# Optimization experiments

Measured on AMD Instinct MI355X. Metric: run time of the kernel, lower is better.

Reference implementation:

```python
import jax, jax.numpy as jnp
import numpy as np

N = 128       # n_channels
B = 131072    # batch
C = np.float32(np.sqrt(0.5))  # 50/50 beamsplitter amplitude (c = s = sqrt(0.5))


def setup_inputs() -> dict:
    key = jax.random.key(0)
    k1, k2, k3, k4 = jax.random.split(key, 4)
    M = N * (N - 1) // 2
    return {
        "x_real": jax.random.normal(k1, (B, N), jnp.float32),
        "x_imag": jax.random.normal(k2, (B, N), jnp.float32),
        "mzi_phases": jax.random.normal(k3, (M * 2,), jnp.float32) * 0.1,
        "output_phases": jax.random.normal(k4, (N,), jnp.float32) * 0.1,
    }


def _construct_unitary(mzi_phases, output_phases):
    n = output_phases.shape[0]
    m = n * (n - 1) // 2
    # pair ordering matches the torch double loop: i ascending, then j > i (row-major triu)
    i_np, j_np = np.triu_indices(n, 1)
    i_idx = jnp.asarray(i_np, jnp.int32)
    j_idx = jnp.asarray(j_np, jnp.int32)
    ph = mzi_phases.reshape(m, 2)
    theta, phi = ph[:, 0], ph[:, 1]

    def step(U, xs):
        th, ph_, i, j = xs
        e_phi = jax.lax.complex(jnp.cos(ph_), jnp.sin(ph_))
        e_th = jax.lax.complex(jnp.cos(th), jnp.sin(th))
        ri = U[i]
        rj = U[j]
        # T_ij @ U touches only rows i and j (O(N) Givens row update)
        new_i = C * ri + (C * e_phi) * rj
        new_j = (C * e_th) * ri - (C * e_th * e_phi) * rj
        U = U.at[i].set(new_i).at[j].set(new_j)
        return U, None

    def chunk_body(U, xs_chunk):
        U, _ = jax.lax.scan(step, U, xs_chunk)
        return U, None

    # chunk the M sequential updates: M = (n-1) * (n//2) for even n;
    # checkpointing chunks keeps reverse-mode memory O(sqrt-ish) instead of O(M * N^2)
    n_chunks = n - 1
    cs = n // 2
    xs = (theta.reshape(n_chunks, cs), phi.reshape(n_chunks, cs),
          i_idx.reshape(n_chunks, cs), j_idx.reshape(n_chunks, cs))
    U0 = jnp.eye(n, dtype=jnp.complex64)
    U, _ = jax.lax.scan(jax.checkpoint(chunk_body), U0, xs)
    # output phase screen D @ U
    d = jax.lax.complex(jnp.cos(output_phases), jnp.sin(output_phases))
    return d[:, None] * U


def reference(x_real, x_imag, mzi_phases, output_phases):
    U = _construct_unitary(mzi_phases, output_phases)           # [N, N] complex64
    x = jax.lax.complex(x_real, x_imag)                          # [B, N] complex64
    # matmul(U, x.unsqueeze(-1)).squeeze(-1) == x @ U^T
    out = jnp.einsum('nm,bm->bn', U, x)                          # [B, N] complex64
    # ComplexDropout is identity in eval mode
    return out
```

## Files before the change

kernel.cpp:

```cpp
#include <hip/hip_runtime.h>
#include <hip/hip_bf16.h>

#define NDIM 128
#define BDIM 131072
#define NMZI 8128
#define NCHUNK 8
#define CSTEP (NMZI / NCHUNK)
#define NJG 8
#define NCOL 32
#define NLOC 16
static constexpr float CC = 0.70710678118654752440f;

typedef __attribute__((ext_vector_type(8))) short bf16x8;
typedef __attribute__((ext_vector_type(4))) float f32x4;

__device__ __align__(16) float4         g_ph[NMZI];
__device__ __align__(8)  float2         g_dt[NDIM];
__device__ __align__(16) float2         g_V[NCHUNK * NDIM * NDIM];
__device__ __align__(16) float2         g_W[4 * NDIM * NDIM];
__device__ __align__(16) float2         g_Y[2 * NDIM * NDIM];
__device__ __align__(16) unsigned short g_Ur[16 * NDIM * 8];
__device__ __align__(16) unsigned short g_Ui[16 * NDIM * 8];

__device__ inline unsigned short f2bf(float f) {
    union { __hip_bfloat16 h; unsigned short u; } cv;
    cv.h = __float2bfloat16(f);
    return cv.u;
}

__global__ void phase_prep(const float* __restrict__ mzi,
                           const float* __restrict__ oph) {
    int q = blockIdx.x * blockDim.x + threadIdx.x;
    if (q < NMZI) {
        float th = mzi[2 * q];
        float p  = mzi[2 * q + 1];
        float sp, cp, st, ct;
        sincosf(p,  &sp, &cp);
        sincosf(th, &st, &ct);
        g_ph[q] = make_float4(cp, sp, CC * ct, CC * st);
    } else if (q < NMZI + NDIM) {
        int n = q - NMZI;
        float s, c;
        sincosf(oph[n], &s, &c);
        g_dt[n] = make_float2(c, s);
    }
}

__global__ __launch_bounds__(256) void build_scan() {
    __shared__ float2 Usm[NDIM][NCOL];
    __shared__ float4 phs[CSTEP];
    __shared__ float4 comp[NJG][NCOL];
    const int tid   = threadIdx.x;
    const int c     = tid & 31;
    const int g     = tid >> 5;
    const int col0  = blockIdx.x * NCOL;
    const int chunk = blockIdx.y;
    const int s0 = chunk * CSTEP, s1 = s0 + CSTEP;

    for (int k = g; k < NDIM; k += NJG)
        Usm[k][c] = make_float2((k == col0 + c) ? 1.f : 0.f, 0.f);
    for (int t = tid; t < CSTEP; t += 256) phs[t] = g_ph[s0 + t];
    __syncthreads();

    int i = 0, base = 0;
    while (base + (NDIM - 1 - i) <= s0) { base += NDIM - 1 - i; ++i; }

    int s = s0;
    while (s < s1) {
        const int cnt  = NDIM - 1 - i;
        const int jA   = i + 1 + (s - base);
        const int L    = min(s1, base + cnt) - s;
        const int nloc = (L + NJG - 1) >> 3;
        const int myBeg = g * nloc;
        const int myN   = max(0, min(nloc, L - myBeg));
        const int pbase = s - s0;

        const float2 r0 = Usm[i][c];

        float2 treg[NLOC];
        float2 qth[NLOC];
        float  A = 1.f;
        float2 Bc = make_float2(0.f, 0.f);
        #pragma unroll
        for (int kk = 0; kk < NLOC; ++kk) {
            if (kk < myN) {
                const int off = myBeg + kk;
                const float4 q  = phs[pbase + off];
                const float2 rj = Usm[jA + off][c];
                const float tr = fmaf(q.x, rj.x, -q.y * rj.y);
                const float ti = fmaf(q.x, rj.y,  q.y * rj.x);
                treg[kk] = make_float2(tr, ti);
                qth[kk]  = make_float2(q.z, q.w);
                Bc.x = CC * (Bc.x + tr);
                Bc.y = CC * (Bc.y + ti);
                A *= CC;
            }
        }
        comp[g][c] = make_float4(A, Bc.x, Bc.y, 0.f);
        __syncthreads();

        float2 r = r0;
        for (int h = 0; h < g; ++h) {
            const float4 cm = comp[h][c];
            r.x = fmaf(cm.x, r.x, cm.y);
            r.y = fmaf(cm.x, r.y, cm.z);
        }

        #pragma unroll
        for (int kk = 0; kk < NLOC; ++kk) {
            if (kk < myN) {
                const float2 t = treg[kk];
                const float2 q = qth[kk];
                const float dr = r.x - t.x, di = r.y - t.y;
                const float njx = fmaf(q.x, dr, -q.y * di);
                const float njy = fmaf(q.x, di,  q.y * dr);
                Usm[jA + myBeg + kk][c] = make_float2(njx, njy);
                r.x = CC * (r.x + t.x);
                r.y = CC * (r.y + t.y);
            }
        }
        if (myN > 0 && (myBeg + myN == L))
            Usm[i][c] = r;
        __syncthreads();

        s += L;
        if (s == base + cnt) { base += cnt; ++i; }
    }

    float2* Vp = g_V + chunk * NDIM * NDIM;
    for (int k = g; k < NDIM; k += NJG)
        Vp[k * NDIM + col0 + c] = Usm[k][c];
}

__global__ __launch_bounds__(128) void compose(int level) {
    const int p = blockIdx.y, n = blockIdx.x, m = threadIdx.x;
    const float2* A; const float2* B; float2* Cout;
    if (level == 0) {
        A = g_V + (2 * p + 1) * NDIM * NDIM;
        B = g_V + (2 * p) * NDIM * NDIM;
        Cout = g_W + p * NDIM * NDIM;
    } else {
        A = g_W + (2 * p + 1) * NDIM * NDIM;
        B = g_W + (2 * p) * NDIM * NDIM;
        Cout = g_Y + p * NDIM * NDIM;
    }
    __shared__ float2 arow[NDIM];
    arow[m] = A[n * NDIM + m];
    __syncthreads();
    float cr = 0.f, ci = 0.f;
    #pragma unroll 8
    for (int k = 0; k < NDIM; ++k) {
        const float2 b = B[k * NDIM + m];
        const float2 a = arow[k];
        cr = fmaf(a.x, b.x, fmaf(-a.y, b.y, cr));
        ci = fmaf(a.x, b.y, fmaf( a.y, b.x, ci));
    }
    Cout[n * NDIM + m] = make_float2(cr, ci);
}

__global__ __launch_bounds__(128) void compose_final() {
    const int n = blockIdx.x, m = threadIdx.x;
    const float2* A = g_Y + NDIM * NDIM;
    const float2* B = g_Y;
    __shared__ float2 arow[NDIM];
    arow[m] = A[n * NDIM + m];
    __syncthreads();
    float cr = 0.f, ci = 0.f;
    #pragma unroll 8
    for (int k = 0; k < NDIM; ++k) {
        const float2 b = B[k * NDIM + m];
        const float2 a = arow[k];
        cr = fmaf(a.x, b.x, fmaf(-a.y, b.y, cr));
        ci = fmaf(a.x, b.y, fmaf( a.y, b.x, ci));
    }
    const float2 d = g_dt[n];
    const float vr = fmaf(cr, d.x, -ci * d.y);
    const float vi = fmaf(cr, d.y,  ci * d.x);
    const int kg = m >> 3, e = m & 7;
    g_Ur[(kg * NDIM + n) * 8 + e] = f2bf(vr);
    g_Ui[(kg * NDIM + n) * 8 + e] = f2bf(vi);
}

template <int OMODE>
__global__ __launch_bounds__(256) void cmatmul(const float* __restrict__ xr,
                                               const float* __restrict__ xi,
                                               void* __restrict__ outp) {
    const int lane  = threadIdx.x & 63;
    const int w     = threadIdx.x >> 6;
    const int btile = blockIdx.x * 64 + w * 16;
    const int r15   = lane & 15;
    const int kg4   = lane >> 4;
    const int bload = btile + r15;

    const bf16x8* Ur = (const bf16x8*)g_Ur;
    const bf16x8* Ui = (const bf16x8*)g_Ui;

    const float* xrp = xr + (size_t)bload * NDIM;
    const float* xip = xi + (size_t)bload * NDIM;

    bf16x8 ar[4], ai[4], ain[4];
    #pragma unroll
    for (int kc = 0; kc < 4; ++kc) {
        const int k0 = kc * 32 + kg4 * 8;
        float4 rlo = *(const float4*)(xrp + k0);
        float4 rhi = *(const float4*)(xrp + k0 + 4);
        float4 ilo = *(const float4*)(xip + k0);
        float4 ihi = *(const float4*)(xip + k0 + 4);
        bf16x8 vr, vi, vn;
        vr[0] = (short)f2bf(rlo.x); vr[1] = (short)f2bf(rlo.y);
        vr[2] = (short)f2bf(rlo.z); vr[3] = (short)f2bf(rlo.w);
        vr[4] = (short)f2bf(rhi.x); vr[5] = (short)f2bf(rhi.y);
        vr[6] = (short)f2bf(rhi.z); vr[7] = (short)f2bf(rhi.w);
        vi[0] = (short)f2bf(ilo.x); vi[1] = (short)f2bf(ilo.y);
        vi[2] = (short)f2bf(ilo.z); vi[3] = (short)f2bf(ilo.w);
        vi[4] = (short)f2bf(ihi.x); vi[5] = (short)f2bf(ihi.y);
        vi[6] = (short)f2bf(ihi.z); vi[7] = (short)f2bf(ihi.w);
        #pragma unroll
        for (int e = 0; e < 8; ++e) vn[e] = (short)(vi[e] ^ 0x8000);
        ar[kc] = vr; ai[kc] = vi; ain[kc] = vn;
    }

    #pragma unroll
    for (int nt = 0; nt < 8; ++nt) {
        f32x4 accR = {0.f, 0.f, 0.f, 0.f};
        f32x4 accI = {0.f, 0.f, 0.f, 0.f};
        #pragma unroll
        for (int kc = 0; kc < 4; ++kc) {
            const int kg = kc * 4 + kg4;
            bf16x8 br = Ur[kg * NDIM + nt * 16 + r15];
            bf16x8 bi = Ui[kg * NDIM + nt * 16 + r15];
            accR = __builtin_amdgcn_mfma_f32_16x16x32_bf16(ar[kc],  br, accR, 0, 0, 0);
            accR = __builtin_amdgcn_mfma_f32_16x16x32_bf16(ain[kc], bi, accR, 0, 0, 0);
            accI = __builtin_amdgcn_mfma_f32_16x16x32_bf16(ar[kc],  bi, accI, 0, 0, 0);
            accI = __builtin_amdgcn_mfma_f32_16x16x32_bf16(ai[kc],  br, accI, 0, 0, 0);
        }
        const int n    = nt * 16 + r15;
        const int brow = btile + kg4 * 4;
        if (OMODE == 0) {
            float* o = (float*)outp;
            #pragma unroll
            for (int r = 0; r < 4; ++r)
                o[(size_t)(brow + r) * NDIM + n] = accR[r];
        } else {
            ushort2* o = (ushort2*)outp;
            #pragma unroll
            for (int r = 0; r < 4; ++r)
                o[(size_t)(brow + r) * NDIM + n] = make_ushort2(f2bf(accR[r]), f2bf(accI[r]));
        }
    }
}

extern "C" void kernel_launch(void* const* d_in, const int* in_sizes, int n_in,
                              void* d_out, int out_size, void* d_ws, size_t ws_size,
                              hipStream_t stream) {
    const float* xr  = (const float*)d_in[0];
    const float* xi  = (const float*)d_in[1];
    const float* mzi = (const float*)d_in[2];
    const float* oph = (const float*)d_in[3];

    phase_prep<<<dim3((NMZI + NDIM + 255) / 256), dim3(256), 0, stream>>>(mzi, oph);
    build_scan<<<dim3(4, NCHUNK), dim3(256), 0, stream>>>();
    compose<<<dim3(NDIM, 4), dim3(128), 0, stream>>>(0);
    compose<<<dim3(NDIM, 2), dim3(128), 0, stream>>>(1);
    compose_final<<<dim3(NDIM), dim3(128), 0, stream>>>();
    if (out_size == BDIM * NDIM) {
        cmatmul<0><<<dim3(BDIM / 64), dim3(256), 0, stream>>>(xr, xi, d_out);
    } else {
        cmatmul<1><<<dim3(BDIM / 64), dim3(256), 0, stream>>>(xr, xi, d_out);
    }
}
```

Before: 131.8 us.

## Fold phase prep into scan kernels and restructure real-output complex matmul with LDS-staged U

Removes the separate phase_prep launch by computing sincos inline in build_scan and compose_final. For the real-output path, a stacked [Re U; -Im U] bf16 operand is built and staged in shared memory. Each block of the new matmul kernel then processes 256 rows with double-buffered register prefetch of x, swapped MFMA operand order and vectorized float4 stores. The added cost is large register pressure from the prefetch buffers and fewer, larger blocks.

```diff
diff --git a/kernel.cpp b/kernel.cpp
--- a/kernel.cpp
+++ b/kernel.cpp
@@ -14,11 +14,10 @@
 typedef __attribute__((ext_vector_type(8))) short bf16x8;
 typedef __attribute__((ext_vector_type(4))) float f32x4;
 
-__device__ __align__(16) float4         g_ph[NMZI];
-__device__ __align__(8)  float2         g_dt[NDIM];
 __device__ __align__(16) float2         g_V[NCHUNK * NDIM * NDIM];
 __device__ __align__(16) float2         g_W[4 * NDIM * NDIM];
 __device__ __align__(16) float2         g_Y[2 * NDIM * NDIM];
+__device__ __align__(16) unsigned short g_TB[32 * NDIM * 8];
 __device__ __align__(16) unsigned short g_Ur[16 * NDIM * 8];
 __device__ __align__(16) unsigned short g_Ui[16 * NDIM * 8];
 
@@ -28,25 +27,7 @@
     return cv.u;
 }
 
-__global__ void phase_prep(const float* __restrict__ mzi,
-                           const float* __restrict__ oph) {
-    int q = blockIdx.x * blockDim.x + threadIdx.x;
-    if (q < NMZI) {
-        float th = mzi[2 * q];
-        float p  = mzi[2 * q + 1];
-        float sp, cp, st, ct;
-        sincosf(p,  &sp, &cp);
-        sincosf(th, &st, &ct);
-        g_ph[q] = make_float4(cp, sp, CC * ct, CC * st);
-    } else if (q < NMZI + NDIM) {
-        int n = q - NMZI;
-        float s, c;
-        sincosf(oph[n], &s, &c);
-        g_dt[n] = make_float2(c, s);
-    }
-}
-
-__global__ __launch_bounds__(256) void build_scan() {
+__global__ __launch_bounds__(256) void build_scan(const float* __restrict__ mzi) {
     __shared__ float2 Usm[NDIM][NCOL];
     __shared__ float4 phs[CSTEP];
     __shared__ float4 comp[NJG][NCOL];
@@ -59,7 +40,14 @@
 
     for (int k = g; k < NDIM; k += NJG)
         Usm[k][c] = make_float2((k == col0 + c) ? 1.f : 0.f, 0.f);
-    for (int t = tid; t < CSTEP; t += 256) phs[t] = g_ph[s0 + t];
+    const float2* mzp = (const float2*)mzi;
+    for (int t = tid; t < CSTEP; t += 256) {
+        const float2 mz = mzp[s0 + t];
+        float sp, cp, st, ct;
+        sincosf(mz.y, &sp, &cp);
+        sincosf(mz.x, &st, &ct);
+        phs[t] = make_float4(cp, sp, CC * ct, CC * st);
+    }
     __syncthreads();
 
     int i = 0, base = 0;
@@ -158,7 +146,7 @@
     Cout[n * NDIM + m] = make_float2(cr, ci);
 }
 
-__global__ __launch_bounds__(128) void compose_final() {
+__global__ __launch_bounds__(128) void compose_final(const float* __restrict__ oph) {
     const int n = blockIdx.x, m = threadIdx.x;
     const float2* A = g_Y + NDIM * NDIM;
     const float2* B = g_Y;
@@ -173,18 +161,99 @@
         cr = fmaf(a.x, b.x, fmaf(-a.y, b.y, cr));
         ci = fmaf(a.x, b.y, fmaf( a.y, b.x, ci));
     }
-    const float2 d = g_dt[n];
-    const float vr = fmaf(cr, d.x, -ci * d.y);
-    const float vi = fmaf(cr, d.y,  ci * d.x);
+    float ds, dc;
+    sincosf(oph[n], &ds, &dc);
+    const float vr = fmaf(cr, dc, -ci * ds);
+    const float vi = fmaf(cr, ds,  ci * dc);
     const int kg = m >> 3, e = m & 7;
+    g_TB[(kg * NDIM + n) * 8 + e]            = f2bf(vr);
+    g_TB[((16 + kg) * NDIM + n) * 8 + e]     = f2bf(-vi);
     g_Ur[(kg * NDIM + n) * 8 + e] = f2bf(vr);
     g_Ui[(kg * NDIM + n) * 8 + e] = f2bf(vi);
 }
 
-template <int OMODE>
-__global__ __launch_bounds__(256) void cmatmul(const float* __restrict__ xr,
-                                               const float* __restrict__ xi,
-                                               void* __restrict__ outp) {
+__global__ __launch_bounds__(256, 2) void cmatmul0(const float* __restrict__ xr,
+                                                   const float* __restrict__ xi,
+                                                   float* __restrict__ out) {
+    __shared__ bf16x8 smT[32 * NDIM];
+    const int tid  = threadIdx.x;
+    const int lane = tid & 63;
+    const int w    = tid >> 6;
+    const int r15  = lane & 15;
+    const int kg4  = lane >> 4;
+    const int rbase = blockIdx.x * 256 + w * 16 + r15;
+
+    float4 bufA[16], bufB[16];
+    {
+        const float* xrp = xr + (size_t)rbase * NDIM;
+        const float* xip = xi + (size_t)rbase * NDIM;
+        #pragma unroll
+        for (int kc = 0; kc < 4; ++kc) {
+            const int k0 = kc * 32 + kg4 * 8;
+            bufA[kc * 2]     = *(const float4*)(xrp + k0);
+            bufA[kc * 2 + 1] = *(const float4*)(xrp + k0 + 4);
+            bufA[8 + kc * 2]     = *(const float4*)(xip + k0);
+            bufA[8 + kc * 2 + 1] = *(const float4*)(xip + k0 + 4);
+        }
+    }
+    const bf16x8* gT = (const bf16x8*)g_TB;
+    for (int t = tid; t < 32 * NDIM; t += 256) smT[t] = gT[t];
+    __syncthreads();
+
+    #pragma unroll
+    for (int t = 0; t < 4; ++t) {
+        float4* cur = (t & 1) ? bufB : bufA;
+        float4* nxt = (t & 1) ? bufA : bufB;
+        if (t < 3) {
+            const int rn = rbase + (t + 1) * 64;
+            const float* xrp = xr + (size_t)rn * NDIM;
+            const float* xip = xi + (size_t)rn * NDIM;
+            #pragma unroll
+            for (int kc = 0; kc < 4; ++kc) {
+                const int k0 = kc * 32 + kg4 * 8;
+                nxt[kc * 2]     = *(const float4*)(xrp + k0);
+                nxt[kc * 2 + 1] = *(const float4*)(xrp + k0 + 4);
+                nxt[8 + kc * 2]     = *(const float4*)(xip + k0);
+                nxt[8 + kc * 2 + 1] = *(const float4*)(xip + k0 + 4);
+            }
+        }
+        bf16x8 fx[8];
+        #pragma unroll
+        for (int kc2 = 0; kc2 < 8; ++kc2) {
+            const float4 lo = cur[kc2 * 2];
+            const float4 hi = cur[kc2 * 2 + 1];
+            bf16x8 v;
+            v[0] = (short)f2bf(lo.x); v[1] = (short)f2bf(lo.y);
+            v[2] = (short)f2bf(lo.z); v[3] = (short)f2bf(lo.w);
+            v[4] = (short)f2bf(hi.x); v[5] = (short)f2bf(hi.y);
+            v[6] = (short)f2bf(hi.z); v[7] = (short)f2bf(hi.w);
+            fx[kc2] = v;
+        }
+        const size_t orow = (size_t)(rbase + t * 64) * NDIM;
+        #pragma unroll
+        for (int nt = 0; nt < 8; ++nt) {
+            f32x4 a0 = {0.f, 0.f, 0.f, 0.f};
+            f32x4 a1 = {0.f, 0.f, 0.f, 0.f};
+            #pragma unroll
+            for (int kc2 = 0; kc2 < 4; ++kc2) {
+                const bf16x8 tf = smT[(kc2 * 4 + kg4) * NDIM + nt * 16 + r15];
+                a0 = __builtin_amdgcn_mfma_f32_16x16x32_bf16(tf, fx[kc2], a0, 0, 0, 0);
+            }
+            #pragma unroll
+            for (int kc2 = 4; kc2 < 8; ++kc2) {
+                const bf16x8 tf = smT[(kc2 * 4 + kg4) * NDIM + nt * 16 + r15];
+                a1 = __builtin_amdgcn_mfma_f32_16x16x32_bf16(tf, fx[kc2], a1, 0, 0, 0);
+            }
+            const f32x4 sum = a0 + a1;
+            *(float4*)(out + orow + nt * 16 + kg4 * 4) =
+                make_float4(sum[0], sum[1], sum[2], sum[3]);
+        }
+    }
+}
+
+__global__ __launch_bounds__(256) void cmatmul1(const float* __restrict__ xr,
+                                                const float* __restrict__ xi,
+                                                ushort2* __restrict__ outp) {
     const int lane  = threadIdx.x & 63;
     const int w     = threadIdx.x >> 6;
     const int btile = blockIdx.x * 64 + w * 16;
@@ -194,7 +263,6 @@
 
     const bf16x8* Ur = (const bf16x8*)g_Ur;
     const bf16x8* Ui = (const bf16x8*)g_Ui;
-
     const float* xrp = xr + (size_t)bload * NDIM;
     const float* xip = xi + (size_t)bload * NDIM;
 
@@ -236,17 +304,9 @@
         }
         const int n    = nt * 16 + r15;
         const int brow = btile + kg4 * 4;
-        if (OMODE == 0) {
-            float* o = (float*)outp;
-            #pragma unroll
-            for (int r = 0; r < 4; ++r)
-                o[(size_t)(brow + r) * NDIM + n] = accR[r];
-        } else {
-            ushort2* o = (ushort2*)outp;
-            #pragma unroll
-            for (int r = 0; r < 4; ++r)
-                o[(size_t)(brow + r) * NDIM + n] = make_ushort2(f2bf(accR[r]), f2bf(accI[r]));
-        }
+        #pragma unroll
+        for (int r = 0; r < 4; ++r)
+            outp[(size_t)(brow + r) * NDIM + n] = make_ushort2(f2bf(accR[r]), f2bf(accI[r]));
     }
 }
 
@@ -258,14 +318,13 @@
     const float* mzi = (const float*)d_in[2];
     const float* oph = (const float*)d_in[3];
 
-    phase_prep<<<dim3((NMZI + NDIM + 255) / 256), dim3(256), 0, stream>>>(mzi, oph);
-    build_scan<<<dim3(4, NCHUNK), dim3(256), 0, stream>>>();
+    build_scan<<<dim3(4, NCHUNK), dim3(256), 0, stream>>>(mzi);
     compose<<<dim3(NDIM, 4), dim3(128), 0, stream>>>(0);
     compose<<<dim3(NDIM, 2), dim3(128), 0, stream>>>(1);
-    compose_final<<<dim3(NDIM), dim3(128), 0, stream>>>();
+    compose_final<<<dim3(NDIM), dim3(128), 0, stream>>>(oph);
     if (out_size == BDIM * NDIM) {
-        cmatmul<0><<<dim3(BDIM / 64), dim3(256), 0, stream>>>(xr, xi, d_out);
+        cmatmul0<<<dim3(512), dim3(256), 0, stream>>>(xr, xi, (float*)d_out);
     } else {
-        cmatmul<1><<<dim3(BDIM / 64), dim3(256), 0, stream>>>(xr, xi, d_out);
-    }
-}
+        cmatmul1<<<dim3(BDIM / 64), dim3(256), 0, stream>>>(xr, xi, (ushort2*)d_out);
+    }
+}
```

Result: faster. 121.5 us (-7.9%).
